# Kernel tuning notes

Measured on AMD Instinct MI355X. Metric: run time of the kernel, lower is better.

Reference implementation:

```python
import jax, jax.numpy as jnp
import numpy as np

N = 4          # BLEU n-gram order
LEN_MAX = 20   # self.len_max
EPS = 1e-9


def _core(tc_res, tc_gts, l_res, l_gts):
    """Clipped n-gram precision pieces for the single hypothesis (r_p_i == 1).
    tc_res: [B, 1, N, K] hypothesis n-gram counts; tc_gts: [B, G, N, K] reference counts;
    l_res: [B, 1], l_gts: [B, G] lengths.
    Returns (g_factor [B,N], und [B,N], l_factor [B])."""
    l_gts = jnp.where(l_gts == 0, LEN_MAX * 10.0, l_gts)            # in-place fixup in torch
    g = tc_res[:, 0]                                                 # [B, N, K]
    l_i = l_res[:, 0]                                                # [B]
    # 'closest' reference-length selection
    idx = jnp.argmin(jnp.abs(l_i[:, None] - l_gts), axis=1)          # [B]
    l_r = jnp.take_along_axis(l_gts, idx[:, None], axis=1)[:, 0]     # [B]
    l_factor = jnp.exp(1.0 - jnp.maximum(1.0 + EPS, (l_r + EPS) / (l_i + EPS)))
    g_gts_max = jnp.max(tc_gts, axis=1)                              # [B, N, K] max over refs
    clipped = jnp.sum(jnp.minimum(g, g_gts_max + EPS), axis=2)       # [B, N]
    # use_bos=True branch: und[:, n] = 1 / (l_i + eps) for every n
    und = jnp.broadcast_to((1.0 / (l_i + EPS))[:, None], clipped.shape)
    return clipped * und, und, l_factor


def reference(tc_res, tc_gts, l_res, l_gts):
    B = tc_res.shape[0]
    g_factor, und, l_factor = _core(tc_res, tc_gts, l_res, l_gts)
    # g_judge: mask of nonzero d(sum g_factor)/d(tc_res) -- the autograd side-channel
    g_judge = jax.grad(lambda t: jnp.sum(_core(t, tc_gts, l_res, l_gts)[0]))(tc_res) != 0
    # 3^N perturbation grid: each n-gram order is {unchanged, +und, relu(-und)}
    ch = jnp.stack([g_factor, g_factor + und, jax.nn.relu(g_factor - und)])   # [3, B, N]
    g_delta = jnp.einsum('ib,jb,kb,lb->bijkl',
                         ch[:, :, 0], ch[:, :, 1], ch[:, :, 2], ch[:, :, 3])  # [B,3,3,3,3]
    flat = g_delta.reshape(B, 3 ** N)
    c_full = l_factor[:, None] * flat ** (1.0 / N)                   # geometric mean * brevity
    c_delta = c_full - c_full[:, -1:]                                # subtract all-minus1 cell
    score_list = c_delta.reshape(B, 1, 3, 3, 3, 3)
    score = c_full[:, 0:1]                                           # c = c_delta_list_[:, 0]
    # score_dif_l: d(loss)/d(l_res); the 3^N block was under torch.no_grad -> detached
    def loss_fn(l_res_):
        gf, _, lf = _core(tc_res, tc_gts, l_res_, l_gts)
        base = jax.lax.stop_gradient(jnp.prod(gf, axis=1))           # == flat[:, 0], detached
        return jnp.sum(lf * base ** (1.0 / N))
    score_dif_l = jax.grad(loss_fn)(l_res)                           # [B, 1]
    return score, score_list, g_judge, score_dif_l


def setup_inputs() -> dict:
    key = jax.random.key(0)
    k1, k2, k3, k4 = jax.random.split(key, 4)
    B, G = 16384, 5
    K = (G + 1) * LEN_MAX + 1  # 121, key_length from process()
    tc_res = jax.random.randint(k1, (B, 1, N, K), 0, 4).astype(jnp.float32)
    tc_gts = jax.random.randint(k2, (B, G, N, K), 0, 4).astype(jnp.float32)
    l_res = jax.random.randint(k3, (B, 1), 1, LEN_MAX + 1).astype(jnp.float32)
    l_gts = jax.random.randint(k4, (B, G), 0, LEN_MAX + 1).astype(jnp.float32)
    return {"tc_res": tc_res, "tc_gts": tc_gts, "l_res": l_res, "l_gts": l_gts}
```

## Files before the change

kernel.cpp:

```cpp
#include <hip/hip_runtime.h>

#define NGRAM 4
#define KDIM 121
#define GDIM 5
#define FEPS 1e-9f
#define NKDIM (NGRAM * KDIM)
#define GNKDIM (GDIM * NKDIM)
#define NCOMBO 81
#define NV4 121

__device__ __forceinline__ float pick3(int s, float x0, float x1, float x2) {
    return (s == 0) ? x0 : ((s == 1) ? x1 : x2);
}

__global__ __launch_bounds__(256, 8) void bleu_kernel(
    const float* __restrict__ tc_res,
    const float* __restrict__ tc_gts,
    const float* __restrict__ l_res,
    const float* __restrict__ l_gts,
    float* __restrict__ o_score,
    float* __restrict__ o_slist,
    float* __restrict__ o_judge,
    float* __restrict__ o_sdl,
    int B)
{
    const int tid  = threadIdx.x;
    const int half = tid >> 7;
    const int t2   = tid & 127;
    const int lane = tid & 63;
    const int wv   = (tid >> 6) & 1;
    const int b    = blockIdx.x * 2 + half;
    const bool valid = (b < B);

    float a0 = 0.0f, a1 = 0.0f, a2 = 0.0f, a3 = 0.0f;

    if (valid && t2 < NV4) {
        const float4* __restrict__ res4 = (const float4*)(tc_res + (size_t)b * NKDIM);
        const float4* __restrict__ gts4 = (const float4*)(tc_gts + (size_t)b * GNKDIM);
        const int vi = t2;

        const float4 g  = res4[vi];
        const float4 m0 = gts4[0 * NV4 + vi];
        const float4 m1 = gts4[1 * NV4 + vi];
        const float4 m2 = gts4[2 * NV4 + vi];
        const float4 m3 = gts4[3 * NV4 + vi];
        const float4 m4 = gts4[4 * NV4 + vi];

        const float mx = fmaxf(fmaxf(fmaxf(m0.x, m1.x), fmaxf(m2.x, m3.x)), m4.x) + FEPS;
        const float my = fmaxf(fmaxf(fmaxf(m0.y, m1.y), fmaxf(m2.y, m3.y)), m4.y) + FEPS;
        const float mz = fmaxf(fmaxf(fmaxf(m0.z, m1.z), fmaxf(m2.z, m3.z)), m4.z) + FEPS;
        const float mw = fmaxf(fmaxf(fmaxf(m0.w, m1.w), fmaxf(m2.w, m3.w)), m4.w) + FEPS;

        float4 j;
        j.x = (g.x <= mx) ? 1.0f : 0.0f;
        j.y = (g.y <= my) ? 1.0f : 0.0f;
        j.z = (g.z <= mz) ? 1.0f : 0.0f;
        j.w = (g.w <= mw) ? 1.0f : 0.0f;
        ((float4*)(o_judge + (size_t)b * NKDIM))[vi] = j;

        const float cx = fminf(g.x, mx);
        const float cy = fminf(g.y, my);
        const float cz = fminf(g.z, mz);
        const float cw = fminf(g.w, mw);

        const int idx = vi * 4;
        const int n0 = (idx >= KDIM) + (idx >= 2 * KDIM) + (idx >= 3 * KDIM);
        const int n3 = (idx + 3 >= KDIM) + (idx + 3 >= 2 * KDIM) + (idx + 3 >= 3 * KDIM);
        if (n0 == n3) {
            const float s = (cx + cy) + (cz + cw);
            a0 += (n0 == 0) ? s : 0.0f;
            a1 += (n0 == 1) ? s : 0.0f;
            a2 += (n0 == 2) ? s : 0.0f;
            a3 += (n0 == 3) ? s : 0.0f;
        } else {
            const float ce[4] = { cx, cy, cz, cw };
            #pragma unroll
            for (int e = 0; e < 4; ++e) {
                const int ie = idx + e;
                const int ne = (ie >= KDIM) + (ie >= 2 * KDIM) + (ie >= 3 * KDIM);
                const float v = ce[e];
                a0 += (ne == 0) ? v : 0.0f;
                a1 += (ne == 1) ? v : 0.0f;
                a2 += (ne == 2) ? v : 0.0f;
                a3 += (ne == 3) ? v : 0.0f;
            }
        }
    }

    #pragma unroll
    for (int s = 1; s < 64; s <<= 1) {
        a0 += __shfl_xor(a0, s, 64);
        a1 += __shfl_xor(a1, s, 64);
        a2 += __shfl_xor(a2, s, 64);
        a3 += __shfl_xor(a3, s, 64);
    }

    __shared__ float4 red[2][2];
    if (lane == 0) red[half][wv] = make_float4(a0, a1, a2, a3);
    __syncthreads();
    const float4 r0 = red[half][0];
    const float4 r1 = red[half][1];
    const float s0 = r0.x + r1.x;
    const float s1 = r0.y + r1.y;
    const float s2 = r0.z + r1.z;
    const float s3 = r0.w + r1.w;

    if (!valid) return;

    const float l_i = l_res[b];
    float best_d = 1e30f;
    float l_r = 0.0f;
    #pragma unroll
    for (int g = 0; g < GDIM; ++g) {
        float lg = l_gts[(size_t)b * GDIM + g];
        lg = (lg == 0.0f) ? 200.0f : lg;
        const float d = fabsf(l_i - lg);
        if (d < best_d) { best_d = d; l_r = lg; }
    }

    const float li_e = l_i + FEPS;
    const float und = 1.0f / li_e;
    const float r = (l_r + FEPS) / li_e;
    const float lf = expf(1.0f - fmaxf(1.0f, r));

    const float gf0 = s0 * und;
    const float gf1 = s1 * und;
    const float gf2 = s2 * und;
    const float gf3 = s3 * und;

    const float c00 = gf0, c01 = gf1, c02 = gf2, c03 = gf3;
    const float c10 = gf0 + und, c11 = gf1 + und, c12 = gf2 + und, c13 = gf3 + und;
    const float c20 = fmaxf(gf0 - und, 0.0f);
    const float c21 = fmaxf(gf1 - und, 0.0f);
    const float c22 = fmaxf(gf2 - und, 0.0f);
    const float c23 = fmaxf(gf3 - und, 0.0f);

    const float p_last = c20 * c21 * c22 * c23;
    const float cf_last = lf * sqrtf(sqrtf(p_last));

    if (t2 < NCOMBO) {
        const int c = t2;
        const int i = c / 27;
        const int j = (c / 9) % 3;
        const int kk = (c / 3) % 3;
        const int l = c % 3;
        const float p = pick3(i, c00, c10, c20) *
                        pick3(j, c01, c11, c21) *
                        pick3(kk, c02, c12, c22) *
                        pick3(l, c03, c13, c23);
        const float cf = lf * sqrtf(sqrtf(p));
        o_slist[(size_t)b * NCOMBO + c] = cf - cf_last;
        if (c == 0) {
            o_score[b] = cf;
            const float base = gf0 * gf1 * gf2 * gf3;
            const float w = (r > 1.0f) ? 1.0f : ((r == 1.0f) ? 0.5f : 0.0f);
            o_sdl[b] = sqrtf(sqrtf(base)) * lf * w * (l_r + FEPS) / (li_e * li_e);
        }
    }
}

extern "C" void kernel_launch(void* const* d_in, const int* in_sizes, int n_in,
                              void* d_out, int out_size, void* d_ws, size_t ws_size,
                              hipStream_t stream) {
    const float* tc_res = (const float*)d_in[0];
    const float* tc_gts = (const float*)d_in[1];
    const float* l_res  = (const float*)d_in[2];
    const float* l_gts  = (const float*)d_in[3];
    const int B = in_sizes[2];

    float* out = (float*)d_out;
    float* o_score = out;
    float* o_slist = o_score + B;
    float* o_judge = o_slist + (size_t)B * NCOMBO;
    float* o_sdl   = o_judge + (size_t)B * NKDIM;

    const int blocks = (B + 1) / 2;
    bleu_kernel<<<blocks, 256, 0, stream>>>(tc_res, tc_gts, l_res, l_gts,
                                            o_score, o_slist, o_judge, o_sdl, B);
}
```

Baseline: 41.32 us.

## Process four rows per block half with register double-buffered prefetch

Each half-block now handles four consecutive batch rows instead of one, and loads the next row's inputs into registers while computing the current row. The aim is to hide global-load latency within a thread and to amortise block launch overhead, with blocks reduced by a factor of four. The cost is higher register pressure (launch bounds lowered to 4) and far fewer blocks in flight, which can cut memory-level parallelism on a bandwidth-bound kernel. The reduction buffer is double-buffered so only one barrier is needed per iteration.

```diff
diff --git a/kernel.cpp b/kernel.cpp
--- a/kernel.cpp
+++ b/kernel.cpp
@@ -8,12 +8,14 @@
 #define GNKDIM (GDIM * NKDIM)
 #define NCOMBO 81
 #define NV4 121
+#define ITERS 4
+#define CHUNK (2 * ITERS)
 
 __device__ __forceinline__ float pick3(int s, float x0, float x1, float x2) {
     return (s == 0) ? x0 : ((s == 1) ? x1 : x2);
 }
 
-__global__ __launch_bounds__(256, 8) void bleu_kernel(
+__global__ __launch_bounds__(256, 4) void bleu_kernel(
     const float* __restrict__ tc_res,
     const float* __restrict__ tc_gts,
     const float* __restrict__ l_res,
@@ -29,133 +31,178 @@
     const int t2   = tid & 127;
     const int lane = tid & 63;
     const int wv   = (tid >> 6) & 1;
-    const int b    = blockIdx.x * 2 + half;
-    const bool valid = (b < B);
-
-    float a0 = 0.0f, a1 = 0.0f, a2 = 0.0f, a3 = 0.0f;
-
-    if (valid && t2 < NV4) {
-        const float4* __restrict__ res4 = (const float4*)(tc_res + (size_t)b * NKDIM);
-        const float4* __restrict__ gts4 = (const float4*)(tc_gts + (size_t)b * GNKDIM);
-        const int vi = t2;
-
-        const float4 g  = res4[vi];
-        const float4 m0 = gts4[0 * NV4 + vi];
-        const float4 m1 = gts4[1 * NV4 + vi];
-        const float4 m2 = gts4[2 * NV4 + vi];
-        const float4 m3 = gts4[3 * NV4 + vi];
-        const float4 m4 = gts4[4 * NV4 + vi];
-
-        const float mx = fmaxf(fmaxf(fmaxf(m0.x, m1.x), fmaxf(m2.x, m3.x)), m4.x) + FEPS;
-        const float my = fmaxf(fmaxf(fmaxf(m0.y, m1.y), fmaxf(m2.y, m3.y)), m4.y) + FEPS;
-        const float mz = fmaxf(fmaxf(fmaxf(m0.z, m1.z), fmaxf(m2.z, m3.z)), m4.z) + FEPS;
-        const float mw = fmaxf(fmaxf(fmaxf(m0.w, m1.w), fmaxf(m2.w, m3.w)), m4.w) + FEPS;
-
-        float4 j;
-        j.x = (g.x <= mx) ? 1.0f : 0.0f;
-        j.y = (g.y <= my) ? 1.0f : 0.0f;
-        j.z = (g.z <= mz) ? 1.0f : 0.0f;
-        j.w = (g.w <= mw) ? 1.0f : 0.0f;
-        ((float4*)(o_judge + (size_t)b * NKDIM))[vi] = j;
-
-        const float cx = fminf(g.x, mx);
-        const float cy = fminf(g.y, my);
-        const float cz = fminf(g.z, mz);
-        const float cw = fminf(g.w, mw);
-
-        const int idx = vi * 4;
-        const int n0 = (idx >= KDIM) + (idx >= 2 * KDIM) + (idx >= 3 * KDIM);
-        const int n3 = (idx + 3 >= KDIM) + (idx + 3 >= 2 * KDIM) + (idx + 3 >= 3 * KDIM);
-        if (n0 == n3) {
-            const float s = (cx + cy) + (cz + cw);
-            a0 += (n0 == 0) ? s : 0.0f;
-            a1 += (n0 == 1) ? s : 0.0f;
-            a2 += (n0 == 2) ? s : 0.0f;
-            a3 += (n0 == 3) ? s : 0.0f;
-        } else {
-            const float ce[4] = { cx, cy, cz, cw };
+
+    const int gbase = blockIdx.x * CHUNK + half * ITERS;
+
+    __shared__ float4 red[2][2][2];
+
+    float4 cg, c0, c1, c2, c3, c4;
+    float cl_i = 1.0f, clg0 = 0.f, clg1 = 0.f, clg2 = 0.f, clg3 = 0.f, clg4 = 0.f;
+
+    {
+        const int b = gbase;
+        if (b < B) {
+            if (t2 < NV4) {
+                const float4* res4 = (const float4*)(tc_res + (size_t)b * NKDIM);
+                const float4* gts4 = (const float4*)(tc_gts + (size_t)b * GNKDIM);
+                cg = res4[t2];
+                c0 = gts4[0 * NV4 + t2];
+                c1 = gts4[1 * NV4 + t2];
+                c2 = gts4[2 * NV4 + t2];
+                c3 = gts4[3 * NV4 + t2];
+                c4 = gts4[4 * NV4 + t2];
+            }
+            cl_i = l_res[b];
+            clg0 = l_gts[(size_t)b * GDIM + 0];
+            clg1 = l_gts[(size_t)b * GDIM + 1];
+            clg2 = l_gts[(size_t)b * GDIM + 2];
+            clg3 = l_gts[(size_t)b * GDIM + 3];
+            clg4 = l_gts[(size_t)b * GDIM + 4];
+        }
+    }
+
+    #pragma unroll
+    for (int it = 0; it < ITERS; ++it) {
+        const int b  = gbase + it;
+        const int bn = gbase + it + 1;
+
+        float4 ng, n0, n1, n2, n3, n4;
+        float nl_i = 1.0f, nlg0 = 0.f, nlg1 = 0.f, nlg2 = 0.f, nlg3 = 0.f, nlg4 = 0.f;
+        if (it + 1 < ITERS && bn < B) {
+            if (t2 < NV4) {
+                const float4* res4 = (const float4*)(tc_res + (size_t)bn * NKDIM);
+                const float4* gts4 = (const float4*)(tc_gts + (size_t)bn * GNKDIM);
+                ng = res4[t2];
+                n0 = gts4[0 * NV4 + t2];
+                n1 = gts4[1 * NV4 + t2];
+                n2 = gts4[2 * NV4 + t2];
+                n3 = gts4[3 * NV4 + t2];
+                n4 = gts4[4 * NV4 + t2];
+            }
+            nl_i = l_res[bn];
+            nlg0 = l_gts[(size_t)bn * GDIM + 0];
+            nlg1 = l_gts[(size_t)bn * GDIM + 1];
+            nlg2 = l_gts[(size_t)bn * GDIM + 2];
+            nlg3 = l_gts[(size_t)bn * GDIM + 3];
+            nlg4 = l_gts[(size_t)bn * GDIM + 4];
+        }
+
+        float a0 = 0.0f, a1 = 0.0f, a2 = 0.0f, a3 = 0.0f;
+        if (b < B && t2 < NV4) {
+            const float mx = fmaxf(fmaxf(fmaxf(c0.x, c1.x), fmaxf(c2.x, c3.x)), c4.x) + FEPS;
+            const float my = fmaxf(fmaxf(fmaxf(c0.y, c1.y), fmaxf(c2.y, c3.y)), c4.y) + FEPS;
+            const float mz = fmaxf(fmaxf(fmaxf(c0.z, c1.z), fmaxf(c2.z, c3.z)), c4.z) + FEPS;
+            const float mw = fmaxf(fmaxf(fmaxf(c0.w, c1.w), fmaxf(c2.w, c3.w)), c4.w) + FEPS;
+
+            float4 j;
+            j.x = (cg.x <= mx) ? 1.0f : 0.0f;
+            j.y = (cg.y <= my) ? 1.0f : 0.0f;
+            j.z = (cg.z <= mz) ? 1.0f : 0.0f;
+            j.w = (cg.w <= mw) ? 1.0f : 0.0f;
+            ((float4*)(o_judge + (size_t)b * NKDIM))[t2] = j;
+
+            const float cx = fminf(cg.x, mx);
+            const float cy = fminf(cg.y, my);
+            const float cz = fminf(cg.z, mz);
+            const float cw = fminf(cg.w, mw);
+
+            const int idx = t2 * 4;
+            const int n0i = (idx >= KDIM) + (idx >= 2 * KDIM) + (idx >= 3 * KDIM);
+            const int n3i = (idx + 3 >= KDIM) + (idx + 3 >= 2 * KDIM) + (idx + 3 >= 3 * KDIM);
+            if (n0i == n3i) {
+                const float s = (cx + cy) + (cz + cw);
+                a0 += (n0i == 0) ? s : 0.0f;
+                a1 += (n0i == 1) ? s : 0.0f;
+                a2 += (n0i == 2) ? s : 0.0f;
+                a3 += (n0i == 3) ? s : 0.0f;
+            } else {
+                const float ce[4] = { cx, cy, cz, cw };
+                #pragma unroll
+                for (int e = 0; e < 4; ++e) {
+                    const int ie = idx + e;
+                    const int ne = (ie >= KDIM) + (ie >= 2 * KDIM) + (ie >= 3 * KDIM);
+                    const float v = ce[e];
+                    a0 += (ne == 0) ? v : 0.0f;
+                    a1 += (ne == 1) ? v : 0.0f;
+                    a2 += (ne == 2) ? v : 0.0f;
+                    a3 += (ne == 3) ? v : 0.0f;
+                }
+            }
+        }
+
+        #pragma unroll
+        for (int s = 1; s < 64; s <<= 1) {
+            a0 += __shfl_xor(a0, s, 64);
+            a1 += __shfl_xor(a1, s, 64);
+            a2 += __shfl_xor(a2, s, 64);
+            a3 += __shfl_xor(a3, s, 64);
+        }
+
+        const int p = it & 1;
+        if (lane == 0) red[p][half][wv] = make_float4(a0, a1, a2, a3);
+        __syncthreads();
+        const float4 r0 = red[p][half][0];
+        const float4 r1 = red[p][half][1];
+        const float s0 = r0.x + r1.x;
+        const float s1 = r0.y + r1.y;
+        const float s2 = r0.z + r1.z;
+        const float s3 = r0.w + r1.w;
+
+        if (b < B) {
+            float best_d = 1e30f;
+            float l_r = 0.0f;
+            const float lgs[GDIM] = { clg0, clg1, clg2, clg3, clg4 };
             #pragma unroll
-            for (int e = 0; e < 4; ++e) {
-                const int ie = idx + e;
-                const int ne = (ie >= KDIM) + (ie >= 2 * KDIM) + (ie >= 3 * KDIM);
-                const float v = ce[e];
-                a0 += (ne == 0) ? v : 0.0f;
-                a1 += (ne == 1) ? v : 0.0f;
-                a2 += (ne == 2) ? v : 0.0f;
-                a3 += (ne == 3) ? v : 0.0f;
-            }
-        }
-    }
-
-    #pragma unroll
-    for (int s = 1; s < 64; s <<= 1) {
-        a0 += __shfl_xor(a0, s, 64);
-        a1 += __shfl_xor(a1, s, 64);
-        a2 += __shfl_xor(a2, s, 64);
-        a3 += __shfl_xor(a3, s, 64);
-    }
-
-    __shared__ float4 red[2][2];
-    if (lane == 0) red[half][wv] = make_float4(a0, a1, a2, a3);
-    __syncthreads();
-    const float4 r0 = red[half][0];
-    const float4 r1 = red[half][1];
-    const float s0 = r0.x + r1.x;
-    const float s1 = r0.y + r1.y;
-    const float s2 = r0.z + r1.z;
-    const float s3 = r0.w + r1.w;
-
-    if (!valid) return;
-
-    const float l_i = l_res[b];
-    float best_d = 1e30f;
-    float l_r = 0.0f;
-    #pragma unroll
-    for (int g = 0; g < GDIM; ++g) {
-        float lg = l_gts[(size_t)b * GDIM + g];
-        lg = (lg == 0.0f) ? 200.0f : lg;
-        const float d = fabsf(l_i - lg);
-        if (d < best_d) { best_d = d; l_r = lg; }
-    }
-
-    const float li_e = l_i + FEPS;
-    const float und = 1.0f / li_e;
-    const float r = (l_r + FEPS) / li_e;
-    const float lf = expf(1.0f - fmaxf(1.0f, r));
-
-    const float gf0 = s0 * und;
-    const float gf1 = s1 * und;
-    const float gf2 = s2 * und;
-    const float gf3 = s3 * und;
-
-    const float c00 = gf0, c01 = gf1, c02 = gf2, c03 = gf3;
-    const float c10 = gf0 + und, c11 = gf1 + und, c12 = gf2 + und, c13 = gf3 + und;
-    const float c20 = fmaxf(gf0 - und, 0.0f);
-    const float c21 = fmaxf(gf1 - und, 0.0f);
-    const float c22 = fmaxf(gf2 - und, 0.0f);
-    const float c23 = fmaxf(gf3 - und, 0.0f);
-
-    const float p_last = c20 * c21 * c22 * c23;
-    const float cf_last = lf * sqrtf(sqrtf(p_last));
-
-    if (t2 < NCOMBO) {
-        const int c = t2;
-        const int i = c / 27;
-        const int j = (c / 9) % 3;
-        const int kk = (c / 3) % 3;
-        const int l = c % 3;
-        const float p = pick3(i, c00, c10, c20) *
-                        pick3(j, c01, c11, c21) *
-                        pick3(kk, c02, c12, c22) *
-                        pick3(l, c03, c13, c23);
-        const float cf = lf * sqrtf(sqrtf(p));
-        o_slist[(size_t)b * NCOMBO + c] = cf - cf_last;
-        if (c == 0) {
-            o_score[b] = cf;
-            const float base = gf0 * gf1 * gf2 * gf3;
-            const float w = (r > 1.0f) ? 1.0f : ((r == 1.0f) ? 0.5f : 0.0f);
-            o_sdl[b] = sqrtf(sqrtf(base)) * lf * w * (l_r + FEPS) / (li_e * li_e);
-        }
+            for (int g = 0; g < GDIM; ++g) {
+                float lg = lgs[g];
+                lg = (lg == 0.0f) ? 200.0f : lg;
+                const float d = fabsf(cl_i - lg);
+                if (d < best_d) { best_d = d; l_r = lg; }
+            }
+
+            const float li_e = cl_i + FEPS;
+            const float und = 1.0f / li_e;
+            const float r = (l_r + FEPS) / li_e;
+            const float lf = expf(1.0f - fmaxf(1.0f, r));
+
+            const float gf0 = s0 * und;
+            const float gf1 = s1 * und;
+            const float gf2 = s2 * und;
+            const float gf3 = s3 * und;
+
+            const float c00 = gf0, c01 = gf1, c02 = gf2, c03 = gf3;
+            const float c10 = gf0 + und, c11 = gf1 + und, c12 = gf2 + und, c13 = gf3 + und;
+            const float c20 = fmaxf(gf0 - und, 0.0f);
+            const float c21 = fmaxf(gf1 - und, 0.0f);
+            const float c22 = fmaxf(gf2 - und, 0.0f);
+            const float c23 = fmaxf(gf3 - und, 0.0f);
+
+            const float p_last = c20 * c21 * c22 * c23;
+            const float cf_last = lf * sqrtf(sqrtf(p_last));
+
+            if (t2 < NCOMBO) {
+                const int c = t2;
+                const int i = c / 27;
+                const int j = (c / 9) % 3;
+                const int kk = (c / 3) % 3;
+                const int l = c % 3;
+                const float pr = pick3(i, c00, c10, c20) *
+                                 pick3(j, c01, c11, c21) *
+                                 pick3(kk, c02, c12, c22) *
+                                 pick3(l, c03, c13, c23);
+                const float cf = lf * sqrtf(sqrtf(pr));
+                o_slist[(size_t)b * NCOMBO + c] = cf - cf_last;
+                if (c == 0) {
+                    o_score[b] = cf;
+                    const float base = gf0 * gf1 * gf2 * gf3;
+                    const float w = (r > 1.0f) ? 1.0f : ((r == 1.0f) ? 0.5f : 0.0f);
+                    o_sdl[b] = sqrtf(sqrtf(base)) * lf * w * (l_r + FEPS) / (li_e * li_e);
+                }
+            }
+        }
+
+        cg = ng; c0 = n0; c1 = n1; c2 = n2; c3 = n3; c4 = n4;
+        cl_i = nl_i; clg0 = nlg0; clg1 = nlg1; clg2 = nlg2; clg3 = nlg3; clg4 = nlg4;
     }
 }
 
@@ -174,7 +221,7 @@
     float* o_judge = o_slist + (size_t)B * NCOMBO;
     float* o_sdl   = o_judge + (size_t)B * NKDIM;
 
-    const int blocks = (B + 1) / 2;
+    const int blocks = (B + CHUNK - 1) / CHUNK;
     bleu_kernel<<<blocks, 256, 0, stream>>>(tc_res, tc_gts, l_res, l_gts,
                                             o_score, o_slist, o_judge, o_sdl, B);
 }
```

New measurement: 42.98 us. +4.0%, slower.
